# Kernel optimization log

Hardware: AMD Instinct MI355X
Metric: run time of the kernel (lower is better)

Reference implementation:

```python
import jax, jax.numpy as jnp
import numpy as np

B, M, HID = 4, 4096, 1024
H, HD = 16, 64          # num_heads, head_dim
SEG = 128               # segment_size
DIL = 2                 # dilation_rate
SCALE = HD ** -0.5


def _hilbert_perm(n_side):
    """Linear indices (y*n+x) visited along a Hilbert curve on an n_side x n_side grid."""
    def d2xy(n, d):
        x = y = 0
        t = d
        s = 1
        while s < n:
            rx = 1 & (t // 2)
            ry = 1 & (t ^ rx)
            if ry == 0:
                if rx == 1:
                    x = s - 1 - x
                    y = s - 1 - y
                x, y = y, x
            x += s * rx
            y += s * ry
            t //= 4
            s *= 2
        return x, y
    idx = np.empty(n_side * n_side, dtype=np.int32)
    for d in range(n_side * n_side):
        x, y = d2xy(n_side, d)
        idx[d] = y * n_side + x
    return idx


def setup_inputs() -> dict:
    key = jax.random.key(0)
    k1, k2, k3 = jax.random.split(key, 3)
    x = jax.random.normal(k1, (B, M, HID), dtype=jnp.float32)
    w_qkv = jax.random.normal(k2, (3 * HID, HID), dtype=jnp.float32) * 0.02
    w_out = jax.random.normal(k3, (HID, HID), dtype=jnp.float32) * 0.02
    hilbert_map = jnp.asarray(_hilbert_perm(int(np.sqrt(M))))  # permutation of [0, M)
    return {"x": x, "w_qkv": w_qkv, "w_out": w_out, "hilbert_map": hilbert_map}


def reference(x, w_qkv, w_out, hilbert_map):
    nseg = M // SEG
    # qkv projection (nn.Linear, no bias): [B, M, 3*HID]
    qkv = x @ w_qkv.T
    qkv = qkv.reshape(B, M, 3, H, HD).transpose(2, 0, 3, 1, 4)  # [3, B, H, M, HD]
    # Hilbert reorder along sequence dim
    qkv = qkv[:, :, :, hilbert_map, :]
    q, k, v = qkv[0], qkv[1], qkv[2]
    # segment into blocks of SEG: [B, H, nseg, SEG, HD]
    q = q.reshape(B, H, nseg, SEG, HD)
    k = k.reshape(B, H, nseg, SEG, HD)
    v = v.reshape(B, H, nseg, SEG, HD)
    scores = jnp.einsum("bhnsd,bhntd->bhnst", q, k) * SCALE
    # dilation mask: position is active if (pos % DIL == 0); pair allowed if row OR col active
    active = (jnp.arange(SEG) % DIL) == 0
    mask = active[:, None] | active[None, :]  # [SEG, SEG]
    scores = jnp.where(mask, scores, jnp.float32(-1e30))
    attn = jax.nn.softmax(scores, axis=-1)
    out = jnp.einsum("bhnst,bhntd->bhnsd", attn, v)  # [B, H, nseg, SEG, HD]
    # output stays in Hilbert order (matches custom autograd semantics)
    out = out.reshape(B, H, M, HD).transpose(0, 2, 1, 3).reshape(B, M, HID)
    return out @ w_out.T
```

## Files before the change

kernel.cpp:

```cpp
#include <hip/hip_runtime.h>
#include <stdint.h>


typedef __attribute__((ext_vector_type(8))) short short8;
typedef __attribute__((ext_vector_type(4))) short short4v;
typedef __attribute__((ext_vector_type(4))) float f32x4;

#define DEV __device__ __forceinline__

DEV short f2bf(float f) {
  union { float f; uint32_t u; } x; x.f = f;
  uint32_t r = x.u + 0x7fffu + ((x.u >> 16) & 1u);
  return (short)(r >> 16);
}

DEV short4v pack4(f32x4 v) {
  short4v o = { f2bf(v[0]), f2bf(v[1]), f2bf(v[2]), f2bf(v[3]) };
  return o;
}

DEV void gload_lds16(const void* g, void* l) {
  __builtin_amdgcn_global_load_lds(
      (const __attribute__((address_space(1))) uint32_t*)g,
      (__attribute__((address_space(3))) uint32_t*)l, 16, 0, 0);
}

#define BAR() __builtin_amdgcn_s_barrier()
#define LGKM0() do { asm volatile("s_waitcnt lgkmcnt(0)" ::: "memory"); \
                     __builtin_amdgcn_sched_barrier(0); } while (0)
#define VMC(n) asm volatile("s_waitcnt vmcnt(" #n ")" ::: "memory")

__global__ __launch_bounds__(256) void k_gather_cast(
    const float* __restrict__ x, const int* __restrict__ perm, short* __restrict__ xp) {
  const int row = blockIdx.x;
  const int b = row >> 12, pos = row & 4095;
  const int src = (b << 12) + perm[pos];
  const f32x4 v = ((const f32x4*)(x + (size_t)src * 1024))[threadIdx.x];
  ((short4v*)(xp + (size_t)row * 1024))[threadIdx.x] = pack4(v);
}

__global__ __launch_bounds__(256) void k_cast(
    const float* __restrict__ src, short* __restrict__ dst) {
  const int i = blockIdx.x * 256 + threadIdx.x;
  const f32x4 v = ((const f32x4*)src)[i];
  ((short4v*)dst)[i] = pack4(v);
}

template <int EPI, int NBJ>
__global__ __launch_bounds__(512, 2) void k_gemm8(
    const short* __restrict__ A, const short* __restrict__ W, void* __restrict__ Cout) {
  __shared__ __attribute__((aligned(16))) short lds[65536];
  const int tid = threadIdx.x;
  const int lane = tid & 63, w = tid >> 6;
  const int wr = w >> 2, wc = w & 3;
  const int lrow = lane & 15, lg = lane >> 4;

  const int nwg = NBJ * 64;
  const int cpx = nwg >> 3;
  const int bid = blockIdx.x;
  const int sw = (bid & 7) * cpx + (bid >> 3);
  const int bi = sw / NBJ, bj = sw % NBJ;

  const short* Abase = A + (size_t)bi * 256 * 1024;
  const short* Bbase = W + (size_t)bj * 256 * 1024;

  const int c0 = tid, c1 = tid + 512;
  const int sOff0 = (c0 >> 3) * 1024 + (((c0 & 7) ^ ((c0 >> 3) & 7)) * 8);
  const int sOff1 = (c1 >> 3) * 1024 + (((c1 & 7) ^ ((c1 >> 3) & 7)) * 8);
  const int pc0 = lg ^ (lrow & 7), pc1 = (4 + lg) ^ (lrow & 7);

  f32x4 acc[2][2][2][4] = {};
  short8 af[4][2], bfrag[2][2][2];

#define ISSUE(base, half, tile, isB) do {                                   \
    const short* _s = (base) + (half) * (128 * 1024) + (tile) * 64;         \
    short* _d = lds + (((tile) & 1) * 32768) + (isB) * 16384 + (half) * 8192; \
    gload_lds16(_s + sOff0, _d + c0 * 8);                                   \
    gload_lds16(_s + sOff1, _d + c1 * 8);                                   \
  } while (0)

#define LDA(mh) do {                                                        \
    const short* _b = ldsbuf + (mh) * 8192;                                 \
    _Pragma("unroll") for (int mi = 0; mi < 4; ++mi) {                      \
      const short* _r = _b + (wr * 64 + mi * 16 + lrow) * 64;               \
      af[mi][0] = *(const short8*)(_r + pc0 * 8);                           \
      af[mi][1] = *(const short8*)(_r + pc1 * 8); } } while (0)

#define LDB(nh) do {                                                        \
    const short* _b = ldsbuf + 16384 + (nh) * 8192;                         \
    _Pragma("unroll") for (int ni = 0; ni < 2; ++ni) {                      \
      const short* _r = _b + (wc * 32 + ni * 16 + lrow) * 64;               \
      bfrag[nh][ni][0] = *(const short8*)(_r + pc0 * 8);                    \
      bfrag[nh][ni][1] = *(const short8*)(_r + pc1 * 8); } } while (0)

#define MM(mh, nh) do {                                                     \
    _Pragma("unroll") for (int ni = 0; ni < 2; ++ni)                        \
    _Pragma("unroll") for (int mi = 0; mi < 4; ++mi) {                      \
      acc[nh][ni][mh][mi] = __builtin_amdgcn_mfma_f32_16x16x32_bf16(        \
          bfrag[nh][ni][0], af[mi][0], acc[nh][ni][mh][mi], 0, 0, 0);       \
      acc[nh][ni][mh][mi] = __builtin_amdgcn_mfma_f32_16x16x32_bf16(        \
          bfrag[nh][ni][1], af[mi][1], acc[nh][ni][mh][mi], 0, 0, 0); } } while (0)

  ISSUE(Abase, 0, 0, 0); ISSUE(Bbase, 0, 0, 1);
  ISSUE(Abase, 1, 0, 0); ISSUE(Bbase, 1, 0, 1);
  ISSUE(Abase, 0, 1, 0); ISSUE(Bbase, 0, 1, 1);
  ISSUE(Abase, 1, 1, 0);
  VMC(6);
  BAR();

#pragma unroll 2
  for (int t = 0; t < 16; ++t) {
    const short* ldsbuf = lds + ((t & 1) * 32768);
    LDA(0); LDB(0);
    if (t < 15) ISSUE(Bbase, 1, t + 1, 1);
    BAR(); LGKM0();
    __builtin_amdgcn_s_setprio(1); MM(0, 0); __builtin_amdgcn_s_setprio(0);
    BAR();
    LDB(1);
    if (t < 14) ISSUE(Abase, 0, t + 2, 0);
    BAR(); LGKM0();
    __builtin_amdgcn_s_setprio(1); MM(0, 1); __builtin_amdgcn_s_setprio(0);
    BAR();
    LDA(1);
    if (t < 14) ISSUE(Bbase, 0, t + 2, 1);
    BAR(); LGKM0();
    __builtin_amdgcn_s_setprio(1); MM(1, 0); __builtin_amdgcn_s_setprio(0);
    BAR();
    if (t < 14) ISSUE(Abase, 1, t + 2, 0);
    __builtin_amdgcn_s_setprio(1); MM(1, 1); __builtin_amdgcn_s_setprio(0);
    if (t < 14) { VMC(6); } else { VMC(0); }
    BAR();
  }
#undef ISSUE
#undef LDA
#undef LDB
#undef MM

  if (EPI == 0) {
    short* Q = (short*)Cout;
    const int bb = bi >> 4;
    const int posc = (bi & 15) * 256 + wr * 64 + lrow;
#pragma unroll
    for (int nh = 0; nh < 2; ++nh)
#pragma unroll
    for (int ni = 0; ni < 2; ++ni) {
      const int gc0 = bj * 256 + nh * 128 + wc * 32 + ni * 16;
      const int sel = gc0 >> 10, h = (gc0 >> 6) & 15;
      const int dbase = (gc0 & 63) + 4 * lg;
      short* basep = Q + (((size_t)(sel * 4 + bb) * 16 + h) << 18) + dbase;
#pragma unroll
      for (int mh = 0; mh < 2; ++mh)
#pragma unroll
      for (int mi = 0; mi < 4; ++mi) {
        const int pos = posc + mh * 128 + mi * 16;
        *(short4v*)(basep + (size_t)pos * 64) = pack4(acc[nh][ni][mh][mi]);
      }
    }
  } else {
    float* C = (float*)Cout;
#pragma unroll
    for (int nh = 0; nh < 2; ++nh)
#pragma unroll
    for (int ni = 0; ni < 2; ++ni) {
      const int gcb = bj * 256 + nh * 128 + wc * 32 + ni * 16 + 4 * lg;
#pragma unroll
      for (int mh = 0; mh < 2; ++mh)
#pragma unroll
      for (int mi = 0; mi < 4; ++mi) {
        const int gr = bi * 256 + mh * 128 + wr * 64 + mi * 16 + lrow;
        *(f32x4*)(C + (size_t)gr * 1024 + gcb) = acc[nh][ni][mh][mi];
      }
    }
  }
}

__global__ __launch_bounds__(256, 3) void k_attn(
    const short* __restrict__ qkv, short* __restrict__ aout) {
  __shared__ __attribute__((aligned(16))) short smem[24576];
  short* Qs = smem;
  short* Ks = smem + 8192;
  short* Vt = smem + 16384;
  short* Ps = smem;
  const int bid = blockIdx.x;
  const int seg = bid & 31, h = (bid >> 5) & 15, b = bid >> 9;
  const size_t plane = (size_t)4096 * 64;
  const short* qp = qkv + ((size_t)(0 * 4 + b) * 16 + h) * plane + seg * 128 * 64;
  const short* kp = qkv + ((size_t)(1 * 4 + b) * 16 + h) * plane + seg * 128 * 64;
  const short* vp = qkv + ((size_t)(2 * 4 + b) * 16 + h) * plane + seg * 128 * 64;
  const int tid = threadIdx.x, lane = tid & 63, w = tid >> 6;
  const int lrow = lane & 15, lg = lane >> 4;

#pragma unroll
  for (int i = 0; i < 4; ++i) {
    int c = i * 256 + tid;
    int row = c >> 3, ch = c & 7, g = ch ^ (row & 7);
    gload_lds16(qp + row * 64 + g * 8, &Qs[c * 8]);
    gload_lds16(kp + row * 64 + g * 8, &Ks[c * 8]);
  }
#pragma unroll
  for (int i = 0; i < 4; ++i) {
    int c = i * 256 + tid;
    int t = c >> 3, d0 = (c & 7) * 8;
    short8 v = *(const short8*)(vp + t * 64 + d0);
#pragma unroll
    for (int j = 0; j < 8; ++j) {
      int d = d0 + j;
      Vt[d * 128 + (t ^ ((d & 7) * 8))] = v[j];
    }
  }
  __syncthreads();

  f32x4 st[8][2] = {};
  __builtin_amdgcn_s_setprio(1);
#pragma unroll
  for (int kk = 0; kk < 2; ++kk) {
    short8 qb[2];
#pragma unroll
    for (int nb = 0; nb < 2; ++nb) {
      int r = w * 32 + nb * 16 + lrow;
      int pc = (kk * 4 + lg) ^ (r & 7);
      qb[nb] = *(const short8*)&Qs[r * 64 + pc * 8];
    }
#pragma unroll
    for (int na = 0; na < 8; ++na) {
      int r = na * 16 + lrow;
      int pc = (kk * 4 + lg) ^ (r & 7);
      short8 ka = *(const short8*)&Ks[r * 64 + pc * 8];
#pragma unroll
      for (int nb = 0; nb < 2; ++nb)
        st[na][nb] = __builtin_amdgcn_mfma_f32_16x16x32_bf16(ka, qb[nb], st[na][nb], 0, 0, 0);
    }
  }
  __builtin_amdgcn_s_setprio(0);

  float inv_sm[2];
  const int oddS = lrow & 1;
#pragma unroll
  for (int nb = 0; nb < 2; ++nb) {
    float pm = -3.0e38f;
#pragma unroll
    for (int na = 0; na < 8; ++na)
#pragma unroll
      for (int reg = 0; reg < 4; ++reg) {
        float v = st[na][nb][reg] * 0.125f;
        if (oddS && (reg & 1)) v = -1.0e30f;
        st[na][nb][reg] = v;
        pm = fmaxf(pm, v);
      }
    pm = fmaxf(pm, __shfl_xor(pm, 16));
    pm = fmaxf(pm, __shfl_xor(pm, 32));
    float sum = 0.f;
#pragma unroll
    for (int na = 0; na < 8; ++na)
#pragma unroll
      for (int reg = 0; reg < 4; ++reg) {
        float p = __expf(st[na][nb][reg] - pm);
        st[na][nb][reg] = p;
        sum += p;
      }
    sum += __shfl_xor(sum, 16);
    sum += __shfl_xor(sum, 32);
    inv_sm[nb] = 1.0f / sum;
  }

  __syncthreads();

#pragma unroll
  for (int na = 0; na < 8; ++na)
#pragma unroll
    for (int nb = 0; nb < 2; ++nb) {
      const int s = w * 32 + nb * 16 + lrow;
      const int t0 = na * 16 + 4 * lg;
      *(short4v*)&Ps[s * 128 + (((t0 >> 3) ^ (s & 7)) * 8) + (t0 & 7)] =
          pack4(st[na][nb]);
    }
  __syncthreads();

  f32x4 ot[4][2] = {};
  __builtin_amdgcn_s_setprio(1);
#pragma unroll
  for (int kt = 0; kt < 4; ++kt) {
    short8 pa[2];
#pragma unroll
    for (int mi = 0; mi < 2; ++mi) {
      int r = w * 32 + mi * 16 + lrow;
      int pc = (kt * 4 + lg) ^ (r & 7);
      pa[mi] = *(const short8*)&Ps[r * 128 + pc * 8];
    }
#pragma unroll
    for (int dn = 0; dn < 4; ++dn) {
      int d = dn * 16 + lrow;
      int pc = (kt * 4 + lg) ^ (d & 7);
      short8 vb = *(const short8*)&Vt[d * 128 + pc * 8];
#pragma unroll
      for (int mi = 0; mi < 2; ++mi)
        ot[dn][mi] = __builtin_amdgcn_mfma_f32_16x16x32_bf16(vb, pa[mi], ot[dn][mi], 0, 0, 0);
    }
  }
  __builtin_amdgcn_s_setprio(0);

#pragma unroll
  for (int dn = 0; dn < 4; ++dn)
#pragma unroll
    for (int mi = 0; mi < 2; ++mi) {
      const int d0 = dn * 16 + 4 * lg;
      const int pos = seg * 128 + w * 32 + mi * 16 + lrow;
      const float iv = inv_sm[mi];
      f32x4 v = ot[dn][mi];
      f32x4 vs = { v[0] * iv, v[1] * iv, v[2] * iv, v[3] * iv };
      *(short4v*)&aout[(size_t)(b * 4096 + pos) * 1024 + h * 64 + d0] = pack4(vs);
    }
}

extern "C" void kernel_launch(void* const* d_in, const int* in_sizes, int n_in,
                              void* d_out, int out_size, void* d_ws, size_t ws_size,
                              hipStream_t stream) {
  const float* x     = (const float*)d_in[0];
  const float* w_qkv = (const float*)d_in[1];
  const float* w_out = (const float*)d_in[2];
  const int*   perm  = (const int*)d_in[3];

  char* ws = (char*)d_ws;
  short* xp   = (short*)(ws);
  short* wq   = (short*)(ws + 33554432);
  short* wo   = (short*)(ws + 33554432 + 6291456);
  short* qkvb = (short*)(ws + 41943040);
  short* aout = xp;

  k_gather_cast<<<16384, 256, 0, stream>>>(x, perm, xp);
  k_cast<<<3072, 256, 0, stream>>>(w_qkv, wq);
  k_cast<<<1024, 256, 0, stream>>>(w_out, wo);
  k_gemm8<0, 12><<<768, 512, 0, stream>>>(xp, wq, qkvb);
  k_attn<<<2048, 256, 0, stream>>>(qkvb, aout);
  k_gemm8<1, 4><<<256, 512, 0, stream>>>(aout, wo, d_out);
}
```

Baseline: 315.4 us.

## Reorder GEMM prefetch schedule and use smaller-tile kernel for output projection

```diff
diff --git a/kernel.cpp b/kernel.cpp
--- a/kernel.cpp
+++ b/kernel.cpp
@@ -104,31 +104,31 @@
   ISSUE(Abase, 0, 0, 0); ISSUE(Bbase, 0, 0, 1);
   ISSUE(Abase, 1, 0, 0); ISSUE(Bbase, 1, 0, 1);
   ISSUE(Abase, 0, 1, 0); ISSUE(Bbase, 0, 1, 1);
-  ISSUE(Abase, 1, 1, 0);
-  VMC(6);
+  VMC(4);
   BAR();
 
 #pragma unroll 2
   for (int t = 0; t < 16; ++t) {
     const short* ldsbuf = lds + ((t & 1) * 32768);
     LDA(0); LDB(0);
-    if (t < 15) ISSUE(Bbase, 1, t + 1, 1);
+    if (t < 15) ISSUE(Abase, 1, t + 1, 0);
     BAR(); LGKM0();
     __builtin_amdgcn_s_setprio(1); MM(0, 0); __builtin_amdgcn_s_setprio(0);
     BAR();
     LDB(1);
-    if (t < 14) ISSUE(Abase, 0, t + 2, 0);
+    if (t < 15) ISSUE(Bbase, 1, t + 1, 1);
     BAR(); LGKM0();
     __builtin_amdgcn_s_setprio(1); MM(0, 1); __builtin_amdgcn_s_setprio(0);
     BAR();
     LDA(1);
-    if (t < 14) ISSUE(Bbase, 0, t + 2, 1);
+    if (t < 14) ISSUE(Abase, 0, t + 2, 0);
     BAR(); LGKM0();
     __builtin_amdgcn_s_setprio(1); MM(1, 0); __builtin_amdgcn_s_setprio(0);
     BAR();
-    if (t < 14) ISSUE(Abase, 1, t + 2, 0);
+    if (t < 14) ISSUE(Bbase, 0, t + 2, 1);
+    BAR(); LGKM0();
     __builtin_amdgcn_s_setprio(1); MM(1, 1); __builtin_amdgcn_s_setprio(0);
-    if (t < 14) { VMC(6); } else { VMC(0); }
+    if (t < 14) { VMC(4); } else { VMC(0); }
     BAR();
   }
 #undef ISSUE
@@ -170,6 +170,66 @@
         const int gr = bi * 256 + mh * 128 + wr * 64 + mi * 16 + lrow;
         *(f32x4*)(C + (size_t)gr * 1024 + gcb) = acc[nh][ni][mh][mi];
       }
+    }
+  }
+}
+
+__global__ __launch_bounds__(256, 3) void k_gemm_s(
+    const short* __restrict__ A, const short* __restrict__ W, float* __restrict__ C) {
+  __shared__ __attribute__((aligned(16))) short As[128 * 64];
+  __shared__ __attribute__((aligned(16))) short Bs[128 * 64];
+  const int tid = threadIdx.x;
+  const int lane = tid & 63, w = tid >> 6;
+  const int wr = w >> 1, wc = w & 1;
+  const int lrow = lane & 15, lg = lane >> 4;
+  const int bid = blockIdx.x;
+  const int sw = (bid & 7) * 128 + (bid >> 3);
+  const int bi = sw >> 3, bj = sw & 7;
+
+  f32x4 acc[4][4] = {};
+  const size_t arow0 = (size_t)bi * 128;
+  const size_t brow0 = (size_t)bj * 128;
+
+  for (int k0 = 0; k0 < 1024; k0 += 64) {
+    __syncthreads();
+#pragma unroll
+    for (int i = 0; i < 4; ++i) {
+      int c = i * 256 + tid;
+      int row = c >> 3, ch = c & 7, g = ch ^ (row & 7);
+      gload_lds16(A + (arow0 + row) * 1024 + k0 + g * 8, &As[c * 8]);
+      gload_lds16(W + (brow0 + row) * 1024 + k0 + g * 8, &Bs[c * 8]);
+    }
+    __syncthreads();
+#pragma unroll
+    for (int kk = 0; kk < 2; ++kk) {
+      short8 af[4], bf[4];
+#pragma unroll
+      for (int mi = 0; mi < 4; ++mi) {
+        int r = wr * 64 + mi * 16 + lrow;
+        int pc = (kk * 4 + lg) ^ (r & 7);
+        af[mi] = *(const short8*)&As[r * 64 + pc * 8];
+      }
+#pragma unroll
+      for (int ni = 0; ni < 4; ++ni) {
+        int r = wc * 64 + ni * 16 + lrow;
+        int pc = (kk * 4 + lg) ^ (r & 7);
+        bf[ni] = *(const short8*)&Bs[r * 64 + pc * 8];
+      }
+#pragma unroll
+      for (int ni = 0; ni < 4; ++ni)
+#pragma unroll
+        for (int mi = 0; mi < 4; ++mi)
+          acc[ni][mi] = __builtin_amdgcn_mfma_f32_16x16x32_bf16(
+              bf[ni], af[mi], acc[ni][mi], 0, 0, 0);
+    }
+  }
+#pragma unroll
+  for (int ni = 0; ni < 4; ++ni) {
+    const int gcb = bj * 128 + wc * 64 + ni * 16 + 4 * lg;
+#pragma unroll
+    for (int mi = 0; mi < 4; ++mi) {
+      const int gr = bi * 128 + wr * 64 + mi * 16 + lrow;
+      *(f32x4*)(C + (size_t)gr * 1024 + gcb) = acc[ni][mi];
     }
   }
 }
@@ -332,5 +392,5 @@
   k_cast<<<1024, 256, 0, stream>>>(w_out, wo);
   k_gemm8<0, 12><<<768, 512, 0, stream>>>(xp, wq, qkvb);
   k_attn<<<2048, 256, 0, stream>>>(qkvb, aout);
-  k_gemm8<1, 4><<<256, 512, 0, stream>>>(aout, wo, d_out);
-}
+  k_gemm_s<<<1024, 256, 0, stream>>>(aout, wo, (float*)d_out);
+}
```

Result: no change. 321.5 us (+1.9%).
